# Optimization experiments

Measured on AMD Instinct MI355X. Metric: run time of the kernel, lower is better.

Reference implementation:

```python
import jax, jax.numpy as jnp
import numpy as np

N, T, V, C_IN = 32, 300, 25, 64
K, F = 3, 128  # spatial kernel size, output filters


def setup_inputs() -> dict:
    key = jax.random.key(0)
    k1, k2, k3, k4 = jax.random.split(key, 4)
    x = jax.random.normal(k1, (N, T, V, C_IN), dtype=jnp.float32)
    A = jax.random.uniform(k2, (K, V, V), dtype=jnp.float32)
    # Conv2D kernel (t_kernel_size=1, 1, C_in, F*K), HWIO layout
    W = jax.random.normal(k3, (1, 1, C_IN, F * K), dtype=jnp.float32) * (1.0 / np.sqrt(C_IN))
    b = jax.random.normal(k4, (F * K,), dtype=jnp.float32) * 0.01
    return {"x": x, "A": A, "W": W, "b": b}


def reference(x, A, W, b):
    # Conv2D with (1,1) kernel == pointwise channel mixing: (N,T,V,Cin) @ (Cin, F*K)
    h = jnp.einsum('ntvc,cd->ntvd', x, W[0, 0]) + b  # (N, T, V, F*K)
    # Reshape channel dim into (K, F): matches Keras Reshape([t, v, K, c//K])
    h = h.reshape(N, T, V, K, F)
    # Graph aggregation over the K-partition adjacency: ntvkc, kvw -> ntwc
    y = jnp.einsum('ntvkc,kvw->ntwc', h, A)  # (N, T, V, F)
    return y
```

## Files before the change

kernel.cpp:

```cpp
#include <hip/hip_runtime.h>

#define N_ 32
#define T_ 300
#define V_ 25
#define C_ 64
#define F_ 128
#define K_ 3
#define D_ 384
#define TB 2
#define NBLK (N_ * (T_ / TB))

typedef _Float16 f16;
typedef f16  f16x4v __attribute__((ext_vector_type(4)));
typedef f16  f16x8v __attribute__((ext_vector_type(8)));
typedef float f32x4v __attribute__((ext_vector_type(4)));

#define WS_WT 0
#define WS_A2 49152

__global__ void gcn_prep(const float* __restrict__ A, const float* __restrict__ W,
                         f16* __restrict__ Wt, f16* __restrict__ A2) {
    int tid = blockIdx.x * blockDim.x + threadIdx.x;
    if (tid < D_ * C_) {
        int d = tid >> 6, c = tid & 63;
        Wt[tid] = (f16)W[c * D_ + d];
    }
    int t2 = tid - D_ * C_;
    if (t2 >= 0 && t2 < K_ * 32 * 32) {
        int k = t2 >> 10, r = t2 & 1023, w = r >> 5, v = r & 31;
        float val = (w < V_ && v < V_) ? A[(k * V_ + v) * V_ + w] : 0.0f;
        A2[t2] = (f16)val;
    }
}

__global__ __launch_bounds__(256, 3) void gcn_fused(
    const float* __restrict__ x, const f16* __restrict__ Wt,
    const f16* __restrict__ A2g, const float* __restrict__ b,
    float* __restrict__ y)
{
    __shared__ __align__(16) f16 x_lds[64][72];
    __shared__ __align__(16) f16 hT_lds[2][128 * 64];
    __shared__ __align__(16) f16 A2_lds[K_ * 32 * 32];

    const int tid  = threadIdx.x;
    const int lane = tid & 63;
    const int wave = tid >> 6;
    const int l15  = lane & 15;
    const int lgr  = lane >> 4;
    const int koff = lgr * 8;

    const int n  = blockIdx.x / (T_ / TB);
    const int t0 = (blockIdx.x % (T_ / TB)) * TB;

    #pragma unroll
    for (int i = 0; i < 2; ++i) {
        int idx = tid + i * 256;
        if (idx < 384) ((uint4*)A2_lds)[idx] = ((const uint4*)A2g)[idx];
    }

    {
        const float4* xs = (const float4*)(x + ((size_t)n * T_ + t0) * (V_ * C_));
        #pragma unroll
        for (int i = 0; i < 4; ++i) {
            int idx = tid + i * 256;
            if (idx < TB * V_ * C_ / 4) {
                float4 v4 = xs[idx];
                int e = idx * 4;
                int t = e / (V_ * C_);
                int r = e - t * (V_ * C_);
                int v = r >> 6, c = r & 63;
                f16x4v hv;
                hv[0] = (f16)v4.x; hv[1] = (f16)v4.y; hv[2] = (f16)v4.z; hv[3] = (f16)v4.w;
                *(f16x4v*)&x_lds[t * 32 + v][c] = hv;
            }
        }
    }
    if (tid < TB * 7 * C_ / 4) {
        int e = tid * 4;
        int t = e / (7 * C_);
        int r = e - t * (7 * C_);
        int v = 25 + (r >> 6), c = r & 63;
        f16x4v z = {(f16)0.f, (f16)0.f, (f16)0.f, (f16)0.f};
        *(f16x4v*)&x_lds[t * 32 + v][c] = z;
    }

    float bias[K_][2];
    #pragma unroll
    for (int k = 0; k < K_; ++k)
        #pragma unroll
        for (int nt = 0; nt < 2; ++nt)
            bias[k][nt] = b[k * F_ + wave * 32 + nt * 16 + l15];

    const f16* wrow = Wt + (size_t)(wave * 32 + l15) * C_ + koff;
    f16x8v wfrA[2][2], wfrB[2][2];
    #pragma unroll
    for (int nt = 0; nt < 2; ++nt)
        #pragma unroll
        for (int kt = 0; kt < 2; ++kt) {
            wfrA[nt][kt] = *(const f16x8v*)(wrow + (size_t)(0 * F_ + nt * 16) * C_ + kt * 32);
            wfrB[nt][kt] = *(const f16x8v*)(wrow + (size_t)(1 * F_ + nt * 16) * C_ + kt * 32);
        }

    f32x4v zero4 = {0.f, 0.f, 0.f, 0.f};
    f32x4v acc2[2][4];
    #pragma unroll
    for (int mt = 0; mt < 2; ++mt)
        #pragma unroll
        for (int nt = 0; nt < 4; ++nt)
            acc2[mt][nt] = zero4;

    const int t  = wave >> 1;
    const int nh = (wave & 1) * 4;

    __syncthreads();

    auto gemm1 = [&](const f16x8v wfr[2][2], const float bk[2], f16* __restrict__ buf) {
        f16x8v xa[4][2];
        #pragma unroll
        for (int mt = 0; mt < 4; ++mt) {
            const f16* xr = &x_lds[mt * 16 + l15][koff];
            xa[mt][0] = *(const f16x8v*)(xr);
            xa[mt][1] = *(const f16x8v*)(xr + 32);
        }
        f32x4v acc1[4][2];
        #pragma unroll
        for (int mt = 0; mt < 4; ++mt)
            #pragma unroll
            for (int nt = 0; nt < 2; ++nt)
                acc1[mt][nt] = zero4;
        #pragma unroll
        for (int kt = 0; kt < 2; ++kt)
            #pragma unroll
            for (int mt = 0; mt < 4; ++mt)
                #pragma unroll
                for (int nt = 0; nt < 2; ++nt)
                    acc1[mt][nt] = __builtin_amdgcn_mfma_f32_16x16x32_f16(
                        xa[mt][kt], wfr[nt][kt], acc1[mt][nt], 0, 0, 0);
        char* hb = (char*)buf;
        #pragma unroll
        for (int mt = 0; mt < 4; ++mt)
            #pragma unroll
            for (int nt = 0; nt < 2; ++nt) {
                int d = wave * 32 + nt * 16 + l15;
                float bv = bk[nt];
                f16x4v h4;
                #pragma unroll
                for (int r = 0; r < 4; ++r) h4[r] = (f16)(acc1[mt][nt][r] + bv);
                int off = (d * 128 + (mt * 16 + lgr * 4) * 2) ^ ((d & 7) << 4);
                *(f16x4v*)(hb + off) = h4;
            }
    };

    auto gemm2 = [&](int k, const f16* __restrict__ buf) {
        f16x8v a2f[2];
        #pragma unroll
        for (int mt = 0; mt < 2; ++mt)
            a2f[mt] = *(const f16x8v*)&A2_lds[((k * 32) + mt * 16 + l15) * 32 + koff];
        const char* hb = (const char*)buf;
        #pragma unroll
        for (int nt = 0; nt < 4; ++nt) {
            int f = (nh + nt) * 16 + l15;
            int off = (f * 128 + (t * 32 + koff) * 2) ^ ((f & 7) << 4);
            f16x8v bv = *(const f16x8v*)(hb + off);
            #pragma unroll
            for (int mt = 0; mt < 2; ++mt)
                acc2[mt][nt] = __builtin_amdgcn_mfma_f32_16x16x32_f16(
                    a2f[mt], bv, acc2[mt][nt], 0, 0, 0);
        }
    };

    gemm1(wfrA, bias[0], hT_lds[0]);
    __syncthreads();

    #pragma unroll
    for (int nt = 0; nt < 2; ++nt)
        #pragma unroll
        for (int kt = 0; kt < 2; ++kt)
            wfrA[nt][kt] = *(const f16x8v*)(wrow + (size_t)(2 * F_ + nt * 16) * C_ + kt * 32);

    gemm1(wfrB, bias[1], hT_lds[1]);
    gemm2(0, hT_lds[0]);
    __syncthreads();

    gemm1(wfrA, bias[2], hT_lds[0]);
    gemm2(1, hT_lds[1]);
    __syncthreads();

    gemm2(2, hT_lds[0]);

    {
        float* yr = y + (((size_t)n * T_ + (t0 + t)) * V_) * F_;
        #pragma unroll
        for (int mt = 0; mt < 2; ++mt) {
            int wb = mt * 16 + lgr * 4;
            #pragma unroll
            for (int nt = 0; nt < 4; ++nt) {
                int f = (nh + nt) * 16 + l15;
                #pragma unroll
                for (int r = 0; r < 4; ++r) {
                    int w = wb + r;
                    if (w < V_) {
                        yr[(size_t)w * F_ + f] = acc2[mt][nt][r];
                    }
                }
            }
        }
    }
}

extern "C" void kernel_launch(void* const* d_in, const int* in_sizes, int n_in,
                              void* d_out, int out_size, void* d_ws, size_t ws_size,
                              hipStream_t stream) {
    const float* x = (const float*)d_in[0];
    const float* A = (const float*)d_in[1];
    const float* W = (const float*)d_in[2];
    const float* b = (const float*)d_in[3];
    float* yout = (float*)d_out;

    f16* Wt = (f16*)((char*)d_ws + WS_WT);
    f16* A2 = (f16*)((char*)d_ws + WS_A2);

    const int prep_threads = D_ * C_ + K_ * 32 * 32;
    gcn_prep<<<(prep_threads + 255) / 256, 256, 0, stream>>>(A, W, Wt, A2);
    gcn_fused<<<NBLK, 256, 0, stream>>>(x, Wt, A2, b, yout);
}
```

Before: 59.34 us.

## Single-buffer h tile and read A from global to raise occupancy

Drops the double-buffered h staging buffer and the LDS copy of the adjacency matrix. A fragments are now read directly from global memory, and each K partition's weights are loaded just in time instead of being kept in registers. LDS per block falls from about 39KB to about 25KB, and launch bounds rise from 3 to 6 blocks per CU, so more blocks can hide memory latency. The cost is an extra barrier per partition, since gemm1 of the next partition can no longer overlap gemm2 of the previous one.

```diff
diff --git a/kernel.cpp b/kernel.cpp
--- a/kernel.cpp
+++ b/kernel.cpp
@@ -33,14 +33,13 @@
     }
 }
 
-__global__ __launch_bounds__(256, 3) void gcn_fused(
+__global__ __launch_bounds__(256, 6) void gcn_fused(
     const float* __restrict__ x, const f16* __restrict__ Wt,
     const f16* __restrict__ A2g, const float* __restrict__ b,
     float* __restrict__ y)
 {
     __shared__ __align__(16) f16 x_lds[64][72];
-    __shared__ __align__(16) f16 hT_lds[2][128 * 64];
-    __shared__ __align__(16) f16 A2_lds[K_ * 32 * 32];
+    __shared__ __align__(16) f16 hT_lds[128 * 64];
 
     const int tid  = threadIdx.x;
     const int lane = tid & 63;
@@ -51,12 +50,6 @@
 
     const int n  = blockIdx.x / (T_ / TB);
     const int t0 = (blockIdx.x % (T_ / TB)) * TB;
-
-    #pragma unroll
-    for (int i = 0; i < 2; ++i) {
-        int idx = tid + i * 256;
-        if (idx < 384) ((uint4*)A2_lds)[idx] = ((const uint4*)A2g)[idx];
-    }
 
     {
         const float4* xs = (const float4*)(x + ((size_t)n * T_ + t0) * (V_ * C_));
@@ -91,16 +84,6 @@
         for (int nt = 0; nt < 2; ++nt)
             bias[k][nt] = b[k * F_ + wave * 32 + nt * 16 + l15];
 
-    const f16* wrow = Wt + (size_t)(wave * 32 + l15) * C_ + koff;
-    f16x8v wfrA[2][2], wfrB[2][2];
-    #pragma unroll
-    for (int nt = 0; nt < 2; ++nt)
-        #pragma unroll
-        for (int kt = 0; kt < 2; ++kt) {
-            wfrA[nt][kt] = *(const f16x8v*)(wrow + (size_t)(0 * F_ + nt * 16) * C_ + kt * 32);
-            wfrB[nt][kt] = *(const f16x8v*)(wrow + (size_t)(1 * F_ + nt * 16) * C_ + kt * 32);
-        }
-
     f32x4v zero4 = {0.f, 0.f, 0.f, 0.f};
     f32x4v acc2[2][4];
     #pragma unroll
@@ -111,82 +94,79 @@
 
     const int t  = wave >> 1;
     const int nh = (wave & 1) * 4;
+    const f16* wrow = Wt + (size_t)(wave * 32 + l15) * C_ + koff;
 
     __syncthreads();
 
-    auto gemm1 = [&](const f16x8v wfr[2][2], const float bk[2], f16* __restrict__ buf) {
-        f16x8v xa[4][2];
-        #pragma unroll
-        for (int mt = 0; mt < 4; ++mt) {
-            const f16* xr = &x_lds[mt * 16 + l15][koff];
-            xa[mt][0] = *(const f16x8v*)(xr);
-            xa[mt][1] = *(const f16x8v*)(xr + 32);
-        }
-        f32x4v acc1[4][2];
-        #pragma unroll
-        for (int mt = 0; mt < 4; ++mt)
-            #pragma unroll
-            for (int nt = 0; nt < 2; ++nt)
-                acc1[mt][nt] = zero4;
-        #pragma unroll
-        for (int kt = 0; kt < 2; ++kt)
+    #pragma unroll
+    for (int k = 0; k < K_; ++k) {
+        if (k) __syncthreads();
+
+        f16x8v wfr[2][2];
+        #pragma unroll
+        for (int nt = 0; nt < 2; ++nt)
+            #pragma unroll
+            for (int kt = 0; kt < 2; ++kt)
+                wfr[nt][kt] = *(const f16x8v*)(wrow + (size_t)(k * F_ + nt * 16) * C_ + kt * 32);
+
+        {
+            f16x8v xa[4][2];
+            #pragma unroll
+            for (int mt = 0; mt < 4; ++mt) {
+                const f16* xr = &x_lds[mt * 16 + l15][koff];
+                xa[mt][0] = *(const f16x8v*)(xr);
+                xa[mt][1] = *(const f16x8v*)(xr + 32);
+            }
+            f32x4v acc1[4][2];
             #pragma unroll
             for (int mt = 0; mt < 4; ++mt)
                 #pragma unroll
                 for (int nt = 0; nt < 2; ++nt)
-                    acc1[mt][nt] = __builtin_amdgcn_mfma_f32_16x16x32_f16(
-                        xa[mt][kt], wfr[nt][kt], acc1[mt][nt], 0, 0, 0);
-        char* hb = (char*)buf;
-        #pragma unroll
-        for (int mt = 0; mt < 4; ++mt)
-            #pragma unroll
-            for (int nt = 0; nt < 2; ++nt) {
-                int d = wave * 32 + nt * 16 + l15;
-                float bv = bk[nt];
-                f16x4v h4;
-                #pragma unroll
-                for (int r = 0; r < 4; ++r) h4[r] = (f16)(acc1[mt][nt][r] + bv);
-                int off = (d * 128 + (mt * 16 + lgr * 4) * 2) ^ ((d & 7) << 4);
-                *(f16x4v*)(hb + off) = h4;
-            }
-    };
-
-    auto gemm2 = [&](int k, const f16* __restrict__ buf) {
+                    acc1[mt][nt] = zero4;
+            #pragma unroll
+            for (int kt = 0; kt < 2; ++kt)
+                #pragma unroll
+                for (int mt = 0; mt < 4; ++mt)
+                    #pragma unroll
+                    for (int nt = 0; nt < 2; ++nt)
+                        acc1[mt][nt] = __builtin_amdgcn_mfma_f32_16x16x32_f16(
+                            xa[mt][kt], wfr[nt][kt], acc1[mt][nt], 0, 0, 0);
+            char* hb = (char*)hT_lds;
+            #pragma unroll
+            for (int mt = 0; mt < 4; ++mt)
+                #pragma unroll
+                for (int nt = 0; nt < 2; ++nt) {
+                    int d = wave * 32 + nt * 16 + l15;
+                    float bv = bias[k][nt];
+                    f16x4v h4;
+                    #pragma unroll
+                    for (int r = 0; r < 4; ++r) h4[r] = (f16)(acc1[mt][nt][r] + bv);
+                    int off = (d * 128 + (mt * 16 + lgr * 4) * 2) ^ ((d & 7) << 4);
+                    *(f16x4v*)(hb + off) = h4;
+                }
+        }
+
         f16x8v a2f[2];
         #pragma unroll
         for (int mt = 0; mt < 2; ++mt)
-            a2f[mt] = *(const f16x8v*)&A2_lds[((k * 32) + mt * 16 + l15) * 32 + koff];
-        const char* hb = (const char*)buf;
-        #pragma unroll
-        for (int nt = 0; nt < 4; ++nt) {
-            int f = (nh + nt) * 16 + l15;
-            int off = (f * 128 + (t * 32 + koff) * 2) ^ ((f & 7) << 4);
-            f16x8v bv = *(const f16x8v*)(hb + off);
-            #pragma unroll
-            for (int mt = 0; mt < 2; ++mt)
-                acc2[mt][nt] = __builtin_amdgcn_mfma_f32_16x16x32_f16(
-                    a2f[mt], bv, acc2[mt][nt], 0, 0, 0);
-        }
-    };
-
-    gemm1(wfrA, bias[0], hT_lds[0]);
-    __syncthreads();
-
-    #pragma unroll
-    for (int nt = 0; nt < 2; ++nt)
-        #pragma unroll
-        for (int kt = 0; kt < 2; ++kt)
-            wfrA[nt][kt] = *(const f16x8v*)(wrow + (size_t)(2 * F_ + nt * 16) * C_ + kt * 32);
-
-    gemm1(wfrB, bias[1], hT_lds[1]);
-    gemm2(0, hT_lds[0]);
-    __syncthreads();
-
-    gemm1(wfrA, bias[2], hT_lds[0]);
-    gemm2(1, hT_lds[1]);
-    __syncthreads();
-
-    gemm2(2, hT_lds[0]);
+            a2f[mt] = *(const f16x8v*)(A2g + ((size_t)(k * 32 + mt * 16 + l15) * 32 + koff));
+
+        __syncthreads();
+
+        {
+            const char* hb = (const char*)hT_lds;
+            #pragma unroll
+            for (int nt = 0; nt < 4; ++nt) {
+                int f = (nh + nt) * 16 + l15;
+                int off = (f * 128 + (t * 32 + koff) * 2) ^ ((f & 7) << 4);
+                f16x8v bv = *(const f16x8v*)(hb + off);
+                #pragma unroll
+                for (int mt = 0; mt < 2; ++mt)
+                    acc2[mt][nt] = __builtin_amdgcn_mfma_f32_16x16x32_f16(
+                        a2f[mt], bv, acc2[mt][nt], 0, 0, 0);
+            }
+        }
+    }
 
     {
         float* yr = y + (((size_t)n * T_ + (t0 + t)) * V_) * F_;
```

Result: slower. 137.6 us (+131.9%).
